# Performance work log

Hardware: AMD Instinct MI355X
Metric: run time of the kernel (lower is better)

Reference implementation:

```python
import jax, jax.numpy as jnp
import numpy as np


def _gru(x, W, U, return_sequences):
    """Keras GRU, reset_after=True, recurrent_activation=sigmoid, activation=linear, no bias.
    x: [B,T,D], W: [D,3D] input kernel, U: [D,3D] recurrent kernel."""
    D = U.shape[0]
    xW = jnp.einsum('btd,de->bte', x, W)  # precompute input projections [B,T,3D]

    def step(h, xw_t):
        hu = h @ U  # [B,3D]
        xz, xr, xh = jnp.split(xw_t, 3, axis=-1)
        uz, ur, uh = jnp.split(hu, 3, axis=-1)
        z = jax.nn.sigmoid(xz + uz)          # update gate
        r = jax.nn.sigmoid(xr + ur)          # reset gate
        hh = xh + r * uh                     # candidate, linear activation, reset_after=True
        h_new = z * h + (1.0 - z) * hh
        return h_new, h_new

    h0 = jnp.zeros((x.shape[0], D), dtype=x.dtype)
    hT, hs = jax.lax.scan(step, h0, jnp.swapaxes(xW, 0, 1))  # scan over time
    return jnp.swapaxes(hs, 0, 1) if return_sequences else hT


def setup_inputs() -> dict:
    key = jax.random.key(0)
    ks = jax.random.split(key, 6)
    B, T, D = 16384, 25, 128
    s = 0.05  # keep gate pre-activations in a sane range
    return {
        "x": jax.random.normal(ks[0], (B, T, D), jnp.float32),
        "W1": jax.random.normal(ks[1], (D, 3 * D), jnp.float32) * s,
        "U1": jax.random.normal(ks[2], (D, 3 * D), jnp.float32) * s,
        "W2": jax.random.normal(ks[3], (D, 3 * D), jnp.float32) * s,
        "U2": jax.random.normal(ks[4], (D, 3 * D), jnp.float32) * s,
        "Wout": jax.random.normal(ks[5], (D, D), jnp.float32) * s,
    }


def reference(x, W1, U1, W2, U2, Wout):
    h1 = _gru(x, W1, U1, True)    # [B,T,D]
    h2 = _gru(h1, W2, U2, False)  # [B,D] last state
    return h2 @ Wout              # [B,D]
```

## Files before the change

kernel.cpp:

```cpp
#include <hip/hip_runtime.h>


typedef _Float16 half8 __attribute__((ext_vector_type(8)));
typedef __fp16  fp16x2 __attribute__((ext_vector_type(2)));
typedef __fp16  fp16x4 __attribute__((ext_vector_type(4)));
typedef float    f32x4 __attribute__((ext_vector_type(4)));

#define MFMA(a, b, c) __builtin_amdgcn_mfma_f32_16x16x32_f16((a), (b), (c), 0, 0, 0)

constexpr int T_STEPS = 25;
constexpr int D = 128;
constexpr int NG = 384;
constexpr int BT = 64;
constexpr int SH = 136;

__device__ __forceinline__ float sigm(float v) {
    return __builtin_amdgcn_rcpf(1.0f + __expf(-v));
}

__device__ __forceinline__ half8 pkrtz8(const f32x4 v0, const f32x4 v1) {
    union { fp16x2 h2[4]; half8 h8; } u;
    u.h2[0] = __builtin_amdgcn_cvt_pkrtz(v0.x, v0.y);
    u.h2[1] = __builtin_amdgcn_cvt_pkrtz(v0.z, v0.w);
    u.h2[2] = __builtin_amdgcn_cvt_pkrtz(v1.x, v1.y);
    u.h2[3] = __builtin_amdgcn_cvt_pkrtz(v1.z, v1.w);
    return u.h8;
}

__global__ __attribute__((amdgpu_flat_work_group_size(1024, 1024),
                          amdgpu_waves_per_eu(4, 4)))
void gru2_kernel(
    const float* __restrict__ x, const float* __restrict__ W1,
    const float* __restrict__ U1, const float* __restrict__ W2,
    const float* __restrict__ U2, const float* __restrict__ Wout,
    float* __restrict__ out) {
    __shared__ _Float16 H1[2][BT * SH];
    __shared__ _Float16 H2[2][BT * SH];

    const int tid = threadIdx.x;
    const int w = tid >> 6, lane = tid & 63, l15 = lane & 15, quad = lane >> 4;
    const int layer = w >> 3;
    const int d0 = (w & 7) * 16;
    const int b0 = blockIdx.x * BT;

    half8 wg[3][8];
    {
        const float* Wp = layer ? W2 : W1;
        const float* Up = layer ? U2 : U1;
#pragma unroll
        for (int g = 0; g < 3; ++g) {
            const int c = g * 128 + d0 + l15;
#pragma unroll
            for (int kt = 0; kt < 8; ++kt) {
                const float* src = (kt < 4 ? Wp : Up) + (size_t)((kt & 3) * 32 + quad * 8) * NG + c;
                half8 f;
#pragma unroll
                for (int e = 0; e < 8; ++e) f[e] = (_Float16)src[(size_t)e * NG];
                wg[g][kt] = f;
            }
        }
    }

    for (int idx = tid; idx < BT * SH; idx += 1024) {
        H1[0][idx] = (_Float16)0.f;
        H2[1][idx] = (_Float16)0.f;
    }
    __syncthreads();

#pragma unroll 1
    for (int it = 0; it <= T_STEPS; ++it) {
        const int p = it & 1, q = p ^ 1;
        const bool active = layer ? (it >= 1) : (it < T_STEPS);
        if (active) {
            const _Float16* Hst = layer ? H2[p] : H1[p];
            _Float16* Hout      = layer ? H2[q] : H1[q];
            const _Float16* Hin = H1[p];
#pragma unroll
            for (int nt = 0; nt < 4; ++nt) {
                const int bb = nt * 16 + l15;
                f32x4 cz = {0.f, 0.f, 0.f, 0.f}, cr = {0.f, 0.f, 0.f, 0.f};
                f32x4 cxh = {0.f, 0.f, 0.f, 0.f}, cuh = {0.f, 0.f, 0.f, 0.f};
                if (!layer) {
                    const float* bx = x + ((size_t)(b0 + bb) * T_STEPS + it) * D + quad * 8;
#pragma unroll
                    for (int kt = 0; kt < 4; ++kt) {
                        const f32x4 v0 = *(const f32x4*)(bx + kt * 32);
                        const f32x4 v1 = *(const f32x4*)(bx + kt * 32 + 4);
                        const half8 B = pkrtz8(v0, v1);
                        cz  = MFMA(wg[0][kt], B, cz);
                        cr  = MFMA(wg[1][kt], B, cr);
                        cxh = MFMA(wg[2][kt], B, cxh);
                    }
                } else {
                    const _Float16* bi = Hin + bb * SH + quad * 8;
#pragma unroll
                    for (int kt = 0; kt < 4; ++kt) {
                        const half8 B = *(const half8*)(bi + kt * 32);
                        cz  = MFMA(wg[0][kt], B, cz);
                        cr  = MFMA(wg[1][kt], B, cr);
                        cxh = MFMA(wg[2][kt], B, cxh);
                    }
                }
                {
                    const _Float16* bs = Hst + bb * SH + quad * 8;
#pragma unroll
                    for (int kt = 0; kt < 4; ++kt) {
                        const half8 B = *(const half8*)(bs + kt * 32);
                        cz  = MFMA(wg[0][4 + kt], B, cz);
                        cr  = MFMA(wg[1][4 + kt], B, cr);
                        cuh = MFMA(wg[2][4 + kt], B, cuh);
                    }
                }
                const int hoff = bb * SH + d0 + quad * 4;
                const fp16x4 hp4 = *(const fp16x4*)(Hst + hoff);
                fp16x4 hn4;
#pragma unroll
                for (int i2 = 0; i2 < 4; ++i2) {
                    const float z = sigm(cz[i2]);
                    const float r = sigm(cr[i2]);
                    const float hh = cxh[i2] + r * cuh[i2];
                    hn4[i2] = (__fp16)(hh + z * ((float)hp4[i2] - hh));
                }
                *(fp16x4*)(Hout + hoff) = hn4;
            }
        }
        __syncthreads();
    }

    if (layer) {
        half8 wO[4];
#pragma unroll
        for (int kt = 0; kt < 4; ++kt) {
            half8 f;
#pragma unroll
            for (int e = 0; e < 8; ++e)
                f[e] = (_Float16)Wout[(size_t)(kt * 32 + quad * 8 + e) * D + d0 + l15];
            wO[kt] = f;
        }
#pragma unroll
        for (int nt = 0; nt < 4; ++nt) {
            const _Float16* bp = H2[0] + (nt * 16 + l15) * SH + quad * 8;
            f32x4 acc = {0.f, 0.f, 0.f, 0.f};
#pragma unroll
            for (int kt = 0; kt < 4; ++kt)
                acc = MFMA(wO[kt], *(const half8*)(bp + kt * 32), acc);
            *(f32x4*)(out + (size_t)(b0 + nt * 16 + l15) * D + d0 + quad * 4) = acc;
        }
    }
}

extern "C" void kernel_launch(void* const* d_in, const int* in_sizes, int n_in,
                              void* d_out, int out_size, void* d_ws, size_t ws_size,
                              hipStream_t stream) {
    const float* x    = (const float*)d_in[0];
    const float* W1   = (const float*)d_in[1];
    const float* U1   = (const float*)d_in[2];
    const float* W2   = (const float*)d_in[3];
    const float* U2   = (const float*)d_in[4];
    const float* Wout = (const float*)d_in[5];
    gru2_kernel<<<dim3(16384 / BT), dim3(1024), 0, stream>>>(
        x, W1, U1, W2, U2, Wout, (float*)d_out);
}
```

Baseline: 599.2 us.

## Prefetch next timestep's x into double-buffered LDS staged by all threads

Layer-0 waves previously loaded x straight from global memory inside the recurrent step, and each of the 8 layer-0 waves reread the full 64x128 tile. Now all 1024 threads cooperatively load the next timestep's x tile at the start of each iteration, convert it to fp16 and write it to a double-buffered LDS array once the current step's compute is done. Layer 0 then reads x from LDS the same way layer 1 reads H1. This hides global load latency behind the current step and removes redundant global reads, at the cost of extra shared memory (about 35 KB), which may limit occupancy.

```diff
diff --git a/kernel.cpp b/kernel.cpp
--- a/kernel.cpp
+++ b/kernel.cpp
@@ -36,12 +36,17 @@
     float* __restrict__ out) {
     __shared__ _Float16 H1[2][BT * SH];
     __shared__ _Float16 H2[2][BT * SH];
+    __shared__ _Float16 XH[2][BT * SH];
 
     const int tid = threadIdx.x;
     const int w = tid >> 6, lane = tid & 63, l15 = lane & 15, quad = lane >> 4;
     const int layer = w >> 3;
     const int d0 = (w & 7) * 16;
     const int b0 = blockIdx.x * BT;
+
+    const int srow = tid >> 4;
+    const int scol = (tid & 15) * 8;
+    const float* xsrc = x + ((size_t)(b0 + srow) * T_STEPS) * D + scol;
 
     half8 wg[3][8];
     {
@@ -65,33 +70,34 @@
         H1[0][idx] = (_Float16)0.f;
         H2[1][idx] = (_Float16)0.f;
     }
+    {
+        const f32x4 v0 = *(const f32x4*)(xsrc + 0);
+        const f32x4 v1 = *(const f32x4*)(xsrc + 4);
+        *(half8*)&XH[0][srow * SH + scol] = pkrtz8(v0, v1);
+    }
     __syncthreads();
 
 #pragma unroll 1
     for (int it = 0; it <= T_STEPS; ++it) {
         const int p = it & 1, q = p ^ 1;
+        f32x4 xa, xb;
+        const bool stage = (it + 1 < T_STEPS);
+        if (stage) {
+            const float* px = xsrc + (size_t)(it + 1) * D;
+            xa = *(const f32x4*)(px + 0);
+            xb = *(const f32x4*)(px + 4);
+        }
         const bool active = layer ? (it >= 1) : (it < T_STEPS);
         if (active) {
             const _Float16* Hst = layer ? H2[p] : H1[p];
             _Float16* Hout      = layer ? H2[q] : H1[q];
-            const _Float16* Hin = H1[p];
+            const _Float16* Hin = layer ? H1[p] : XH[p];
 #pragma unroll
             for (int nt = 0; nt < 4; ++nt) {
                 const int bb = nt * 16 + l15;
                 f32x4 cz = {0.f, 0.f, 0.f, 0.f}, cr = {0.f, 0.f, 0.f, 0.f};
                 f32x4 cxh = {0.f, 0.f, 0.f, 0.f}, cuh = {0.f, 0.f, 0.f, 0.f};
-                if (!layer) {
-                    const float* bx = x + ((size_t)(b0 + bb) * T_STEPS + it) * D + quad * 8;
-#pragma unroll
-                    for (int kt = 0; kt < 4; ++kt) {
-                        const f32x4 v0 = *(const f32x4*)(bx + kt * 32);
-                        const f32x4 v1 = *(const f32x4*)(bx + kt * 32 + 4);
-                        const half8 B = pkrtz8(v0, v1);
-                        cz  = MFMA(wg[0][kt], B, cz);
-                        cr  = MFMA(wg[1][kt], B, cr);
-                        cxh = MFMA(wg[2][kt], B, cxh);
-                    }
-                } else {
+                {
                     const _Float16* bi = Hin + bb * SH + quad * 8;
 #pragma unroll
                     for (int kt = 0; kt < 4; ++kt) {
@@ -123,6 +129,9 @@
                 }
                 *(fp16x4*)(Hout + hoff) = hn4;
             }
+        }
+        if (stage) {
+            *(half8*)&XH[q][srow * SH + scol] = pkrtz8(xa, xb);
         }
         __syncthreads();
     }
```

After: 937.7 us. 1.56x slower.
